# Optimization experiments

Measured on AMD Instinct MI355X. Metric: run time of the kernel, lower is better.

The kernel has to match this reference:

```python
import jax, jax.numpy as jnp
import numpy as np

N = 4096          # total nodes
G = 8             # graphs in batch
M_PER = N // G    # nodes per graph (contiguous batch ids)
DEG = 8           # random out-edges per node before symmetrization (~16 after)


def setup_inputs() -> dict:
    rng = np.random.default_rng(0)
    A = np.zeros((N, N), dtype=np.float32)
    for g in range(G):
        lo = g * M_PER
        u = rng.integers(lo, lo + M_PER, size=M_PER * DEG)
        v = rng.integers(lo, lo + M_PER, size=M_PER * DEG)
        A[u, v] = 1.0
        ring = np.arange(lo, lo + M_PER)           # guarantee no isolated nodes
        A[ring, np.roll(ring, -1)] = 1.0
    A = np.maximum(A, A.T)                          # undirected (symmetric)
    np.fill_diagonal(A, 0.0)                        # no self loops
    batch = np.repeat(np.arange(G), M_PER).astype(np.int64)
    return {"A": jnp.asarray(A), "batch": jnp.asarray(batch), "num_graphs": G}


def _netsimile_node_features(A):
    # Vectorized form of the per-node ego-network loop.
    # Row n of M1 is the boolean mask of the 1-hop egonet {n} U N(n);
    # B = M1 @ A counts, for each (n, v), edges from ego1(n) into v, so
    # M2 = M1 | (B > 0) is the 2-hop egonet mask. All loop statistics become
    # row reductions of these matrices.
    n = A.shape[0]
    deg = A.sum(axis=1)                                  # [N] feat0: degree
    deg_safe = jnp.maximum(deg, 1.0)
    f0 = deg
    f2 = jnp.where(deg > 0, (A @ deg) / deg_safe, 0.0)   # scatter_mean(deg[col], row)

    eye = jnp.eye(n, dtype=A.dtype)
    M1 = jnp.maximum(A, eye)                             # [N,N] 1-hop ego masks
    B = M1 @ A                                           # [N,N] one-step reach counts
    f4_raw = (B * M1).sum(axis=1)                        # directed edges inside ego1
    M2 = jnp.maximum(M1, (B > 0).astype(A.dtype))        # [N,N] 2-hop ego masks
    f5 = M2 @ deg - 2.0 * f4_raw                         # sum(mask2[row]) - 2*feat4 (incl. post-loop -=)
    f6 = M2.sum(axis=1) - deg - 1.0                      # |ego2| - deg - 1

    denom = jnp.where(deg > 1, deg * (deg - 1.0), 1.0)
    f1 = jnp.where(deg > 1, (f4_raw - deg) / denom, 0.0)  # clustering coeff
    # undirected graph corrections (data.is_undirected() is True)
    f1 = f1 * 2.0
    f4 = f4_raw / 2.0
    f3 = jnp.where(deg > 0, (A @ f1) / deg_safe, 0.0)     # scatter_mean(f1[col], row)
    return jnp.stack([f0, f1, f2, f3, f4, f5, f6], axis=1)  # [N,7]


def reference(A, batch, num_graphs):
    feat = _netsimile_node_features(A)                   # [N,7]
    n, F = feat.shape
    m = n // num_graphs                                  # equal-size contiguous graphs
    xg = feat.reshape(num_graphs, m, F)                  # batch ids are sorted blocks
    mean = xg.mean(axis=1)                               # [G,7]
    c = xg - mean[:, None, :]
    m2 = (c ** 2).mean(axis=1)
    m3 = (c ** 3).mean(axis=1)
    m4 = (c ** 4).mean(axis=1)
    # torch.median returns the LOWER middle element for even counts
    median = jnp.sort(xg, axis=1)[:, (m - 1) // 2, :]
    eps = jnp.float32(1e-4)
    skew = m3 / jnp.maximum(m2 ** 1.5, eps)
    kurt = m4 / jnp.maximum(m2 ** 2, eps)
    return jnp.hstack([mean, median, jnp.sqrt(m2), skew, kurt])  # [G,35]
```

## Files before the change

kernel.cpp:

```cpp
#include <hip/hip_runtime.h>
#include <stdint.h>

typedef unsigned long long u64;

#define NNODE 4096
#define NG    8
#define M     512
#define W     8

#define OFF_MASK 0
#define OFF_DEG  (262144)
#define OFF_F1   (262144 + 16384)
#define OFF_FEAT (262144 + 32768)

__global__ __launch_bounds__(256) void k_pack(const float* __restrict__ A,
                                              u64* __restrict__ gmask,
                                              float* __restrict__ gdeg) {
    int row  = (blockIdx.x << 2) + (threadIdx.x >> 6);
    int lane = threadIdx.x & 63;
    int lo   = (row >> 9) << 9;
    const float* rowp = A + (size_t)row * NNODE + lo;
    float4 a = *(const float4*)(rowp + lane * 8);
    float4 b = *(const float4*)(rowp + lane * 8 + 4);
    unsigned int byte =
        (a.x != 0.f ? 1u : 0u) | (a.y != 0.f ? 2u : 0u) |
        (a.z != 0.f ? 4u : 0u) | (a.w != 0.f ? 8u : 0u) |
        (b.x != 0.f ? 16u : 0u) | (b.y != 0.f ? 32u : 0u) |
        (b.z != 0.f ? 64u : 0u) | (b.w != 0.f ? 128u : 0u);
    ((unsigned char*)gmask)[(size_t)row * 64 + lane] = (unsigned char)byte;
    int c = __popc(byte);
#pragma unroll
    for (int off = 32; off; off >>= 1) c += __shfl_down(c, off, 64);
    if (lane == 0) gdeg[row] = (float)c;
}

static __device__ __forceinline__ u64 shfl_xor_u64(u64 v, int mask) {
    return ((u64)(unsigned)__shfl_xor((int)(v >> 32), mask, 64) << 32) |
           (u64)(unsigned)__shfl_xor((int)(v & 0xffffffffu), mask, 64);
}

__global__ __launch_bounds__(256) void k_feat(const u64* __restrict__ gmask,
                                              const float* __restrict__ gdeg,
                                              float* __restrict__ featg,
                                              float* __restrict__ f1g) {
    int g = blockIdx.x >> 3, chunk = blockIdx.x & 7;
    int t = threadIdx.x;
    __shared__ u64 smT[W * M];
    __shared__ float sdeg[M];
    __shared__ u64 planes[9][W];

    const u64* gm = gmask + (size_t)g * M * W;
    for (int idx = t; idx < M * W; idx += 256) {
        int u = idx >> 3, w = idx & 7;
        smT[w * M + u] = gm[idx];
    }
    for (int i = t; i < M; i += 256) sdeg[i] = gdeg[g * M + i];
    __syncthreads();

    int wv = t >> 6, lane = t & 63;
    for (int w = wv; w < W; w += 4) {
        int d = (int)sdeg[(w << 6) + lane];
#pragma unroll
        for (int k = 0; k < 9; k++) {
            u64 bal = __ballot(((d >> k) & 1) != 0);
            if (lane == 0) planes[k][w] = bal;
        }
    }
    __syncthreads();

    int nl = t >> 2, q = t & 3;
    int n  = chunk * 64 + nl;
    u64 m1[W], reach[W];
#pragma unroll
    for (int w = 0; w < W; w++) { m1[w] = smT[w * M + n]; reach[w] = 0ull; }
    m1[n >> 6] |= 1ull << (n & 63);

    int f4 = 0;
#pragma unroll
    for (int wq = 0; wq < 2; wq++) {
        int w = 2 * q + wq;
        u64 bits = m1[w];
        while (bits) {
            int b = __ffsll(bits) - 1;
            bits &= bits - 1;
            int u = (w << 6) + b;
#pragma unroll
            for (int w2 = 0; w2 < W; w2++) {
                u64 r = smT[w2 * M + u];
                reach[w2] |= r;
                f4 += __popcll(r & m1[w2]);
            }
        }
    }
    f4 += __shfl_xor(f4, 1, 64);
    f4 += __shfl_xor(f4, 2, 64);
#pragma unroll
    for (int w = 0; w < W; w++) {
        reach[w] |= shfl_xor_u64(reach[w], 1);
        reach[w] |= shfl_xor_u64(reach[w], 2);
    }

    if (q == 0) {
        int f6c = 0;
        u64 m2m[W];
#pragma unroll
        for (int w = 0; w < W; w++) { m2m[w] = m1[w] | reach[w]; f6c += __popcll(m2m[w]); }
        int f5i = 0, f2i = 0;
        u64 arow_self = 1ull << (n & 63);
#pragma unroll
        for (int k = 0; k < 9; k++) {
            int c5 = 0, c2 = 0;
#pragma unroll
            for (int w = 0; w < W; w++) {
                u64 ar = (w == (n >> 6)) ? (m1[w] & ~arow_self) : m1[w];
                c5 += __popcll(m2m[w] & planes[k][w]);
                c2 += __popcll(ar & planes[k][w]);
            }
            f5i += c5 << k;
            f2i += c2 << k;
        }
        float deg = sdeg[n];
        float f4raw = (float)f4;
        float f1 = (deg > 1.f) ? 2.f * (f4raw - deg) / (deg * (deg - 1.f)) : 0.f;
        float* fb = featg + (size_t)g * 7 * M;
        fb[0 * M + n] = deg;
        fb[1 * M + n] = f1;
        fb[2 * M + n] = (deg > 0.f) ? (float)f2i / deg : 0.f;
        fb[4 * M + n] = f4raw * 0.5f;
        fb[5 * M + n] = (float)f5i - 2.f * f4raw;
        fb[6 * M + n] = (float)f6c - deg - 1.f;
        f1g[g * M + n] = f1;
    }
}

__global__ __launch_bounds__(512) void k_f3(const u64* __restrict__ gmask,
                                            const float* __restrict__ gdeg,
                                            const float* __restrict__ f1g,
                                            float* __restrict__ featg) {
    int g = blockIdx.x;
    int t = threadIdx.x;
    __shared__ float f1s[M];
    f1s[t] = f1g[g * M + t];
    __syncthreads();

    const u64* m = gmask + ((size_t)g * M + t) * W;
    float sum = 0.f;
#pragma unroll
    for (int w = 0; w < W; w++) {
        u64 bits = m[w];
        while (bits) {
            int b = __ffsll(bits) - 1;
            bits &= bits - 1;
            sum += f1s[(w << 6) + b];
        }
    }
    float deg = gdeg[g * M + t];
    featg[(size_t)g * 7 * M + 3 * M + t] = (deg > 0.f) ? sum / deg : 0.f;
}

__global__ __launch_bounds__(256) void k_stats(const float* __restrict__ featg,
                                               float* __restrict__ out) {
    int blk = blockIdx.x;
    int gf = blk >> 1, half = blk & 1;
    int g = gf / 7, f = gf % 7;
    int t = threadIdx.x;
    __shared__ __align__(16) float sv[M];
    __shared__ double rsum[4], r2[4], r3[4], r4[4];
    __shared__ double smean;

    sv[t]       = featg[(size_t)gf * M + t];
    sv[t + 256] = featg[(size_t)gf * M + t + 256];
    __syncthreads();

    int wv = t >> 6, lane = t & 63;
    if (half == 0) {
        double s = (double)sv[t] + (double)sv[t + 256];
#pragma unroll
        for (int off = 32; off; off >>= 1) s += __shfl_xor(s, off, 64);
        if (lane == 0) rsum[wv] = s;
        __syncthreads();
        if (t == 0) smean = (rsum[0] + rsum[1] + rsum[2] + rsum[3]) * (1.0 / 512.0);
        __syncthreads();
        double mean = smean;
        double c1 = (double)sv[t] - mean, c2v = (double)sv[t + 256] - mean;
        double a2 = c1 * c1, b2 = c2v * c2v;
        double p2 = a2 + b2, p3 = a2 * c1 + b2 * c2v, p4 = a2 * a2 + b2 * b2;
#pragma unroll
        for (int off = 32; off; off >>= 1) {
            p2 += __shfl_xor(p2, off, 64);
            p3 += __shfl_xor(p3, off, 64);
            p4 += __shfl_xor(p4, off, 64);
        }
        if (lane == 0) { r2[wv] = p2; r3[wv] = p3; r4[wv] = p4; }
        __syncthreads();
        if (t == 0) {
            double m2 = (r2[0] + r2[1] + r2[2] + r2[3]) * (1.0 / 512.0);
            double m3 = (r3[0] + r3[1] + r3[2] + r3[3]) * (1.0 / 512.0);
            double m4 = (r4[0] + r4[1] + r4[2] + r4[3]) * (1.0 / 512.0);
            double sd = sqrt(m2);
            double den3 = m2 * sd;  if (den3 < 1e-4) den3 = 1e-4;
            double den4 = m2 * m2;  if (den4 < 1e-4) den4 = 1e-4;
            out[g * 35 + f]      = (float)smean;
            out[g * 35 + 14 + f] = (float)sd;
            out[g * 35 + 21 + f] = (float)(m3 / den3);
            out[g * 35 + 28 + f] = (float)(m4 / den4);
        }
    }

    float cv = sv[half * 256 + t];
    int less = 0, eq = 0;
    for (int j = 0; j < M; j += 4) {
        float4 x = *(const float4*)&sv[j];
        less += (x.x < cv) + (x.y < cv) + (x.z < cv) + (x.w < cv);
        eq   += (x.x == cv) + (x.y == cv) + (x.z == cv) + (x.w == cv);
    }
    if (less <= 255 && less + eq > 255) out[g * 35 + 7 + f] = cv;
}

extern "C" void kernel_launch(void* const* d_in, const int* in_sizes, int n_in,
                              void* d_out, int out_size, void* d_ws, size_t ws_size,
                              hipStream_t stream) {
    const float* A = (const float*)d_in[0];
    float* out = (float*)d_out;
    char* ws = (char*)d_ws;
    u64*   gmask = (u64*)(ws + OFF_MASK);
    float* gdeg  = (float*)(ws + OFF_DEG);
    float* f1g   = (float*)(ws + OFF_F1);
    float* featg = (float*)(ws + OFF_FEAT);

    k_pack <<<NNODE / 4, 256, 0, stream>>>(A, gmask, gdeg);
    k_feat <<<NG * 8,    256, 0, stream>>>(gmask, gdeg, featg, f1g);
    k_f3   <<<NG,        512, 0, stream>>>(gmask, gdeg, f1g, featg);
    k_stats<<<NG * 7 * 2, 256, 0, stream>>>(featg, out);
}
```

Measured before the change: 114.2 us.

## Fuse four kernels into one cooperative kernel with grid-wide syncs

Replaces the pack, feature, f3 and stats launches with a single cooperative kernel of 256 blocks. The phases are separated by grid.sync(), and each phase is gated by block index. This removes three kernel launch gaps and the idle tails between stages. In exchange it adds grid barrier costs, leaves most blocks idle in the later phases, and raises per-block shared memory, which could limit how many blocks can be co-resident for the cooperative launch.

```diff
diff --git a/kernel.cpp b/kernel.cpp
--- a/kernel.cpp
+++ b/kernel.cpp
@@ -1,6 +1,8 @@
 #include <hip/hip_runtime.h>
+#include <hip/hip_cooperative_groups.h>
 #include <stdint.h>
 
+namespace cg = cooperative_groups;
 typedef unsigned long long u64;
 
 #define NNODE 4096
@@ -13,208 +15,212 @@
 #define OFF_F1   (262144 + 16384)
 #define OFF_FEAT (262144 + 32768)
 
-__global__ __launch_bounds__(256) void k_pack(const float* __restrict__ A,
-                                              u64* __restrict__ gmask,
-                                              float* __restrict__ gdeg) {
-    int row  = (blockIdx.x << 2) + (threadIdx.x >> 6);
-    int lane = threadIdx.x & 63;
-    int lo   = (row >> 9) << 9;
-    const float* rowp = A + (size_t)row * NNODE + lo;
-    float4 a = *(const float4*)(rowp + lane * 8);
-    float4 b = *(const float4*)(rowp + lane * 8 + 4);
-    unsigned int byte =
-        (a.x != 0.f ? 1u : 0u) | (a.y != 0.f ? 2u : 0u) |
-        (a.z != 0.f ? 4u : 0u) | (a.w != 0.f ? 8u : 0u) |
-        (b.x != 0.f ? 16u : 0u) | (b.y != 0.f ? 32u : 0u) |
-        (b.z != 0.f ? 64u : 0u) | (b.w != 0.f ? 128u : 0u);
-    ((unsigned char*)gmask)[(size_t)row * 64 + lane] = (unsigned char)byte;
-    int c = __popc(byte);
-#pragma unroll
-    for (int off = 32; off; off >>= 1) c += __shfl_down(c, off, 64);
-    if (lane == 0) gdeg[row] = (float)c;
-}
-
 static __device__ __forceinline__ u64 shfl_xor_u64(u64 v, int mask) {
     return ((u64)(unsigned)__shfl_xor((int)(v >> 32), mask, 64) << 32) |
            (u64)(unsigned)__shfl_xor((int)(v & 0xffffffffu), mask, 64);
 }
 
-__global__ __launch_bounds__(256) void k_feat(const u64* __restrict__ gmask,
-                                              const float* __restrict__ gdeg,
-                                              float* __restrict__ featg,
-                                              float* __restrict__ f1g) {
-    int g = blockIdx.x >> 3, chunk = blockIdx.x & 7;
-    int t = threadIdx.x;
-    __shared__ u64 smT[W * M];
+__global__ __launch_bounds__(256) void k_fused(const float* __restrict__ A,
+                                               float* __restrict__ out,
+                                               char* __restrict__ ws) {
+    u64*   gmask = (u64*)(ws + OFF_MASK);
+    float* gdeg  = (float*)(ws + OFF_DEG);
+    float* f1g   = (float*)(ws + OFF_F1);
+    float* featg = (float*)(ws + OFF_FEAT);
+
+    cg::grid_group grid = cg::this_grid();
+    int b = blockIdx.x, t = threadIdx.x;
+    int wv = t >> 6, lane = t & 63;
+
+    __shared__ __align__(16) u64 smT[W * M];
     __shared__ float sdeg[M];
     __shared__ u64 planes[9][W];
-
-    const u64* gm = gmask + (size_t)g * M * W;
-    for (int idx = t; idx < M * W; idx += 256) {
-        int u = idx >> 3, w = idx & 7;
-        smT[w * M + u] = gm[idx];
-    }
-    for (int i = t; i < M; i += 256) sdeg[i] = gdeg[g * M + i];
-    __syncthreads();
-
-    int wv = t >> 6, lane = t & 63;
-    for (int w = wv; w < W; w += 4) {
-        int d = (int)sdeg[(w << 6) + lane];
-#pragma unroll
-        for (int k = 0; k < 9; k++) {
-            u64 bal = __ballot(((d >> k) & 1) != 0);
-            if (lane == 0) planes[k][w] = bal;
-        }
-    }
-    __syncthreads();
-
-    int nl = t >> 2, q = t & 3;
-    int n  = chunk * 64 + nl;
-    u64 m1[W], reach[W];
-#pragma unroll
-    for (int w = 0; w < W; w++) { m1[w] = smT[w * M + n]; reach[w] = 0ull; }
-    m1[n >> 6] |= 1ull << (n & 63);
-
-    int f4 = 0;
-#pragma unroll
-    for (int wq = 0; wq < 2; wq++) {
-        int w = 2 * q + wq;
-        u64 bits = m1[w];
-        while (bits) {
-            int b = __ffsll(bits) - 1;
-            bits &= bits - 1;
-            int u = (w << 6) + b;
-#pragma unroll
-            for (int w2 = 0; w2 < W; w2++) {
-                u64 r = smT[w2 * M + u];
-                reach[w2] |= r;
-                f4 += __popcll(r & m1[w2]);
-            }
-        }
-    }
-    f4 += __shfl_xor(f4, 1, 64);
-    f4 += __shfl_xor(f4, 2, 64);
-#pragma unroll
-    for (int w = 0; w < W; w++) {
-        reach[w] |= shfl_xor_u64(reach[w], 1);
-        reach[w] |= shfl_xor_u64(reach[w], 2);
-    }
-
-    if (q == 0) {
-        int f6c = 0;
-        u64 m2m[W];
-#pragma unroll
-        for (int w = 0; w < W; w++) { m2m[w] = m1[w] | reach[w]; f6c += __popcll(m2m[w]); }
-        int f5i = 0, f2i = 0;
-        u64 arow_self = 1ull << (n & 63);
-#pragma unroll
-        for (int k = 0; k < 9; k++) {
-            int c5 = 0, c2 = 0;
+    __shared__ __align__(16) float sv[M];
+    __shared__ double rsum[4], r2s[4], r3s[4], r4s[4];
+    __shared__ double smean;
+
+#pragma unroll
+    for (int k = 0; k < 4; k++) {
+        int row = b * 16 + wv * 4 + k;
+        int lo  = (row >> 9) << 9;
+        const float* rowp = A + (size_t)row * NNODE + lo;
+        float4 a = *(const float4*)(rowp + lane * 8);
+        float4 c4 = *(const float4*)(rowp + lane * 8 + 4);
+        unsigned int byte =
+            (a.x  != 0.f ? 1u : 0u) | (a.y  != 0.f ? 2u : 0u) |
+            (a.z  != 0.f ? 4u : 0u) | (a.w  != 0.f ? 8u : 0u) |
+            (c4.x != 0.f ? 16u : 0u) | (c4.y != 0.f ? 32u : 0u) |
+            (c4.z != 0.f ? 64u : 0u) | (c4.w != 0.f ? 128u : 0u);
+        ((unsigned char*)gmask)[(size_t)row * 64 + lane] = (unsigned char)byte;
+        int c = __popc(byte);
+#pragma unroll
+        for (int off = 32; off; off >>= 1) c += __shfl_down(c, off, 64);
+        if (lane == 0) gdeg[row] = (float)c;
+    }
+    grid.sync();
+
+    if (b < 64) {
+        int g = b >> 3, chunk = b & 7;
+        const u64* gm = gmask + (size_t)g * M * W;
+        for (int idx = t; idx < M * W; idx += 256) {
+            int u = idx >> 3, w = idx & 7;
+            smT[w * M + u] = gm[idx];
+        }
+        for (int i = t; i < M; i += 256) sdeg[i] = gdeg[g * M + i];
+        __syncthreads();
+
+        for (int w = wv; w < W; w += 4) {
+            int d = (int)sdeg[(w << 6) + lane];
+#pragma unroll
+            for (int k = 0; k < 9; k++) {
+                u64 bal = __ballot(((d >> k) & 1) != 0);
+                if (lane == 0) planes[k][w] = bal;
+            }
+        }
+        __syncthreads();
+
+        int nl = t >> 2, q = t & 3;
+        int n  = chunk * 64 + nl;
+        u64 m1[W], reach[W];
+#pragma unroll
+        for (int w = 0; w < W; w++) { m1[w] = smT[w * M + n]; reach[w] = 0ull; }
+        m1[n >> 6] |= 1ull << (n & 63);
+
+        int f4 = 0;
+#pragma unroll
+        for (int wq = 0; wq < 2; wq++) {
+            int w = 2 * q + wq;
+            u64 bits = m1[w];
+            while (bits) {
+                int bb = __ffsll(bits) - 1;
+                bits &= bits - 1;
+                int u = (w << 6) + bb;
+#pragma unroll
+                for (int w2 = 0; w2 < W; w2++) {
+                    u64 r = smT[w2 * M + u];
+                    reach[w2] |= r;
+                    f4 += __popcll(r & m1[w2]);
+                }
+            }
+        }
+        f4 += __shfl_xor(f4, 1, 64);
+        f4 += __shfl_xor(f4, 2, 64);
+#pragma unroll
+        for (int w = 0; w < W; w++) {
+            reach[w] |= shfl_xor_u64(reach[w], 1);
+            reach[w] |= shfl_xor_u64(reach[w], 2);
+        }
+
+        if (q == 0) {
+            int f6c = 0;
+            u64 m2m[W];
+#pragma unroll
+            for (int w = 0; w < W; w++) { m2m[w] = m1[w] | reach[w]; f6c += __popcll(m2m[w]); }
+            int f5i = 0, f2i = 0;
+            u64 selfb = 1ull << (n & 63);
+#pragma unroll
+            for (int k = 0; k < 9; k++) {
+                int c5 = 0, c2 = 0;
+#pragma unroll
+                for (int w = 0; w < W; w++) {
+                    u64 ar = (w == (n >> 6)) ? (m1[w] & ~selfb) : m1[w];
+                    c5 += __popcll(m2m[w] & planes[k][w]);
+                    c2 += __popcll(ar & planes[k][w]);
+                }
+                f5i += c5 << k;
+                f2i += c2 << k;
+            }
+            float deg = sdeg[n];
+            float f4raw = (float)f4;
+            float f1 = (deg > 1.f) ? 2.f * (f4raw - deg) / (deg * (deg - 1.f)) : 0.f;
+            float* fb = featg + (size_t)g * 7 * M;
+            fb[0 * M + n] = deg;
+            fb[1 * M + n] = f1;
+            fb[2 * M + n] = (deg > 0.f) ? (float)f2i / deg : 0.f;
+            fb[4 * M + n] = f4raw * 0.5f;
+            fb[5 * M + n] = (float)f5i - 2.f * f4raw;
+            fb[6 * M + n] = (float)f6c - deg - 1.f;
+            f1g[g * M + n] = f1;
+        }
+    }
+    grid.sync();
+
+    if (b < NG) {
+        int g = b;
+        sv[t]       = f1g[g * M + t];
+        sv[t + 256] = f1g[g * M + t + 256];
+        __syncthreads();
+#pragma unroll
+        for (int h = 0; h < 2; h++) {
+            int n = h * 256 + t;
+            const u64* m = gmask + ((size_t)g * M + n) * W;
+            float sum = 0.f;
 #pragma unroll
             for (int w = 0; w < W; w++) {
-                u64 ar = (w == (n >> 6)) ? (m1[w] & ~arow_self) : m1[w];
-                c5 += __popcll(m2m[w] & planes[k][w]);
-                c2 += __popcll(ar & planes[k][w]);
-            }
-            f5i += c5 << k;
-            f2i += c2 << k;
-        }
-        float deg = sdeg[n];
-        float f4raw = (float)f4;
-        float f1 = (deg > 1.f) ? 2.f * (f4raw - deg) / (deg * (deg - 1.f)) : 0.f;
-        float* fb = featg + (size_t)g * 7 * M;
-        fb[0 * M + n] = deg;
-        fb[1 * M + n] = f1;
-        fb[2 * M + n] = (deg > 0.f) ? (float)f2i / deg : 0.f;
-        fb[4 * M + n] = f4raw * 0.5f;
-        fb[5 * M + n] = (float)f5i - 2.f * f4raw;
-        fb[6 * M + n] = (float)f6c - deg - 1.f;
-        f1g[g * M + n] = f1;
-    }
-}
-
-__global__ __launch_bounds__(512) void k_f3(const u64* __restrict__ gmask,
-                                            const float* __restrict__ gdeg,
-                                            const float* __restrict__ f1g,
-                                            float* __restrict__ featg) {
-    int g = blockIdx.x;
-    int t = threadIdx.x;
-    __shared__ float f1s[M];
-    f1s[t] = f1g[g * M + t];
-    __syncthreads();
-
-    const u64* m = gmask + ((size_t)g * M + t) * W;
-    float sum = 0.f;
-#pragma unroll
-    for (int w = 0; w < W; w++) {
-        u64 bits = m[w];
-        while (bits) {
-            int b = __ffsll(bits) - 1;
-            bits &= bits - 1;
-            sum += f1s[(w << 6) + b];
-        }
-    }
-    float deg = gdeg[g * M + t];
-    featg[(size_t)g * 7 * M + 3 * M + t] = (deg > 0.f) ? sum / deg : 0.f;
-}
-
-__global__ __launch_bounds__(256) void k_stats(const float* __restrict__ featg,
-                                               float* __restrict__ out) {
-    int blk = blockIdx.x;
-    int gf = blk >> 1, half = blk & 1;
-    int g = gf / 7, f = gf % 7;
-    int t = threadIdx.x;
-    __shared__ __align__(16) float sv[M];
-    __shared__ double rsum[4], r2[4], r3[4], r4[4];
-    __shared__ double smean;
-
-    sv[t]       = featg[(size_t)gf * M + t];
-    sv[t + 256] = featg[(size_t)gf * M + t + 256];
-    __syncthreads();
-
-    int wv = t >> 6, lane = t & 63;
-    if (half == 0) {
-        double s = (double)sv[t] + (double)sv[t + 256];
-#pragma unroll
-        for (int off = 32; off; off >>= 1) s += __shfl_xor(s, off, 64);
-        if (lane == 0) rsum[wv] = s;
-        __syncthreads();
-        if (t == 0) smean = (rsum[0] + rsum[1] + rsum[2] + rsum[3]) * (1.0 / 512.0);
-        __syncthreads();
-        double mean = smean;
-        double c1 = (double)sv[t] - mean, c2v = (double)sv[t + 256] - mean;
-        double a2 = c1 * c1, b2 = c2v * c2v;
-        double p2 = a2 + b2, p3 = a2 * c1 + b2 * c2v, p4 = a2 * a2 + b2 * b2;
-#pragma unroll
-        for (int off = 32; off; off >>= 1) {
-            p2 += __shfl_xor(p2, off, 64);
-            p3 += __shfl_xor(p3, off, 64);
-            p4 += __shfl_xor(p4, off, 64);
-        }
-        if (lane == 0) { r2[wv] = p2; r3[wv] = p3; r4[wv] = p4; }
-        __syncthreads();
-        if (t == 0) {
-            double m2 = (r2[0] + r2[1] + r2[2] + r2[3]) * (1.0 / 512.0);
-            double m3 = (r3[0] + r3[1] + r3[2] + r3[3]) * (1.0 / 512.0);
-            double m4 = (r4[0] + r4[1] + r4[2] + r4[3]) * (1.0 / 512.0);
-            double sd = sqrt(m2);
-            double den3 = m2 * sd;  if (den3 < 1e-4) den3 = 1e-4;
-            double den4 = m2 * m2;  if (den4 < 1e-4) den4 = 1e-4;
-            out[g * 35 + f]      = (float)smean;
-            out[g * 35 + 14 + f] = (float)sd;
-            out[g * 35 + 21 + f] = (float)(m3 / den3);
-            out[g * 35 + 28 + f] = (float)(m4 / den4);
-        }
-    }
-
-    float cv = sv[half * 256 + t];
-    int less = 0, eq = 0;
-    for (int j = 0; j < M; j += 4) {
-        float4 x = *(const float4*)&sv[j];
-        less += (x.x < cv) + (x.y < cv) + (x.z < cv) + (x.w < cv);
-        eq   += (x.x == cv) + (x.y == cv) + (x.z == cv) + (x.w == cv);
-    }
-    if (less <= 255 && less + eq > 255) out[g * 35 + 7 + f] = cv;
+                u64 bits = m[w];
+                while (bits) {
+                    int bb = __ffsll(bits) - 1;
+                    bits &= bits - 1;
+                    sum += sv[(w << 6) + bb];
+                }
+            }
+            float deg = gdeg[g * M + n];
+            featg[(size_t)g * 7 * M + 3 * M + n] = (deg > 0.f) ? sum / deg : 0.f;
+        }
+    }
+    grid.sync();
+
+    if (b < NG * 7 * 2) {
+        int gf = b >> 1, half = b & 1;
+        int g = gf / 7, f = gf % 7;
+
+        sv[t]       = featg[(size_t)gf * M + t];
+        sv[t + 256] = featg[(size_t)gf * M + t + 256];
+        __syncthreads();
+
+        if (half == 0) {
+            double s = (double)sv[t] + (double)sv[t + 256];
+#pragma unroll
+            for (int off = 32; off; off >>= 1) s += __shfl_xor(s, off, 64);
+            if (lane == 0) rsum[wv] = s;
+            __syncthreads();
+            if (t == 0) smean = (rsum[0] + rsum[1] + rsum[2] + rsum[3]) * (1.0 / 512.0);
+            __syncthreads();
+            double mean = smean;
+            double c1 = (double)sv[t] - mean, c2v = (double)sv[t + 256] - mean;
+            double a2 = c1 * c1, b2 = c2v * c2v;
+            double p2 = a2 + b2, p3 = a2 * c1 + b2 * c2v, p4 = a2 * a2 + b2 * b2;
+#pragma unroll
+            for (int off = 32; off; off >>= 1) {
+                p2 += __shfl_xor(p2, off, 64);
+                p3 += __shfl_xor(p3, off, 64);
+                p4 += __shfl_xor(p4, off, 64);
+            }
+            if (lane == 0) { r2s[wv] = p2; r3s[wv] = p3; r4s[wv] = p4; }
+            __syncthreads();
+            if (t == 0) {
+                double m2 = (r2s[0] + r2s[1] + r2s[2] + r2s[3]) * (1.0 / 512.0);
+                double m3 = (r3s[0] + r3s[1] + r3s[2] + r3s[3]) * (1.0 / 512.0);
+                double m4 = (r4s[0] + r4s[1] + r4s[2] + r4s[3]) * (1.0 / 512.0);
+                double sd = sqrt(m2);
+                double den3 = m2 * sd;  if (den3 < 1e-4) den3 = 1e-4;
+                double den4 = m2 * m2;  if (den4 < 1e-4) den4 = 1e-4;
+                out[g * 35 + f]      = (float)smean;
+                out[g * 35 + 14 + f] = (float)sd;
+                out[g * 35 + 21 + f] = (float)(m3 / den3);
+                out[g * 35 + 28 + f] = (float)(m4 / den4);
+            }
+        }
+
+        float cv = sv[half * 256 + t];
+        int less = 0, eq = 0;
+        for (int j = 0; j < M; j += 4) {
+            float4 x = *(const float4*)&sv[j];
+            less += (x.x < cv) + (x.y < cv) + (x.z < cv) + (x.w < cv);
+            eq   += (x.x == cv) + (x.y == cv) + (x.z == cv) + (x.w == cv);
+        }
+        if (less <= 255 && less + eq > 255) out[g * 35 + 7 + f] = cv;
+    }
 }
 
 extern "C" void kernel_launch(void* const* d_in, const int* in_sizes, int n_in,
@@ -223,13 +229,8 @@
     const float* A = (const float*)d_in[0];
     float* out = (float*)d_out;
     char* ws = (char*)d_ws;
-    u64*   gmask = (u64*)(ws + OFF_MASK);
-    float* gdeg  = (float*)(ws + OFF_DEG);
-    float* f1g   = (float*)(ws + OFF_F1);
-    float* featg = (float*)(ws + OFF_FEAT);
-
-    k_pack <<<NNODE / 4, 256, 0, stream>>>(A, gmask, gdeg);
-    k_feat <<<NG * 8,    256, 0, stream>>>(gmask, gdeg, featg, f1g);
-    k_f3   <<<NG,        512, 0, stream>>>(gmask, gdeg, f1g, featg);
-    k_stats<<<NG * 7 * 2, 256, 0, stream>>>(featg, out);
+
+    void* args[] = { (void*)&A, (void*)&out, (void*)&ws };
+    hipLaunchCooperativeKernel((const void*)k_fused, dim3(256), dim3(256),
+                               args, 0, stream);
 }
```

New measurement: 205.0 us. +79.5%, slower.
